# Optimization experiments

Hardware: AMD Instinct MI355X
Metric: run time of the kernel (lower is better)

The kernel has to match this reference:

```python
import jax, jax.numpy as jnp
import numpy as np

LN_ZERO = -100000000000.0
F_, D_, C_, V_ = 250000, 4, 2, 250000
E_ = F_ * D_
CD_ = C_ ** D_


def setup_inputs() -> dict:
    key = jax.random.key(0)
    k1, k2, k3 = jax.random.split(key, 3)
    # each factor has exactly D_ incident edges, one per variable slot
    edge_f = np.repeat(np.arange(E_ // D_ * 0 + F_ * 0 + F_)[:F_], D_)  # [E]
    pos = np.tile(np.arange(D_), F_)  # variable slot of each edge within its factor
    edge_v = np.asarray(jax.random.randint(k3, (E_,), 0, V_))
    # digit of each flat factor state along each axis: digits[k, s] in [0, C)
    state = np.arange(CD_)
    digits = (state[None, :] // (C_ ** (D_ - 1 - np.arange(D_)))[:, None]) % C_  # [D, CD]
    s_p = digits[pos]  # [E, CD]: the edge's own variable state within each factor state
    # permutation indices into the broadcast-first layout [E, C, C^(D-1)]
    scatter_idx = (np.arange(E_)[:, None] * CD_ + s_p * C_ ** (D_ - 1)).reshape(-1)
    fac_states_to_var = (np.arange(E_)[:, None] * C_ + s_p).reshape(-1)
    return {
        "prv_factorToVar_messages": jax.random.normal(k1, (E_, C_), jnp.float32),
        "factor_potentials": jax.random.normal(k2, (F_,) + (C_,) * D_, jnp.float32),
        "facToVar_edge_idx": jnp.asarray(np.stack([edge_f, edge_v]), jnp.int32),
        "facStates_to_varIdx": jnp.asarray(fac_states_to_var, jnp.int32),
        "varToFactorMsg_scatter_indices": jnp.asarray(scatter_idx, jnp.int32),
        "factor_potential_masks": jnp.zeros((F_,) + (C_,) * D_, jnp.int32),
        "factorToVar_messages_masks": jnp.zeros((E_, C_), bool),
        "varToFactor_messages_masks": jnp.zeros((E_, C_), bool),
        "var_beliefs_masks": jnp.zeros((V_, C_), bool),
    }


def _mask_clamp(x, mask):
    return jnp.maximum(jnp.where(mask, LN_ZERO, x), LN_ZERO)


def reference(prv_factorToVar_messages, factor_potentials, facToVar_edge_idx,
              facStates_to_varIdx, varToFactorMsg_scatter_indices,
              factor_potential_masks, factorToVar_messages_masks,
              varToFactor_messages_masks, var_beliefs_masks):
    E, C = prv_factorToVar_messages.shape
    F = factor_potentials.shape[0]
    V = var_beliefs_masks.shape[0]
    D = factor_potentials.ndim - 1
    edge_f, edge_v = facToVar_edge_idx[0], facToVar_edge_idx[1]

    def beliefs(msgs):
        vb = _mask_clamp(jax.ops.segment_sum(msgs, edge_v, num_segments=V), var_beliefs_masks)
        v2f = _mask_clamp(vb[edge_v] - msgs, varToFactor_messages_masks)
        # expanded[e, s] = v2f[e, s_p]; source is broadcast layout [E, C, C^(D-1)]
        expanded = v2f.reshape(-1)[varToFactorMsg_scatter_indices // (C ** (D - 1))]
        expanded = expanded.reshape((E,) + (C,) * D)
        fb = jax.ops.segment_sum(expanded.reshape(E, -1), edge_f, num_segments=F)
        fb = fb.reshape(factor_potentials.shape) + factor_potentials
        fb = jnp.maximum(jnp.where(factor_potential_masks == 1, LN_ZERO, fb), LN_ZERO)
        return vb, v2f, expanded, fb

    prv_vb, prv_v2f, exp_prv_v2f, prv_fb = beliefs(prv_factorToVar_messages)

    # new factor->var messages: max-marginalize (mode='map')
    nfv = prv_fb[edge_f] - exp_prv_v2f
    nfv = nfv - jnp.max(nfv)
    flat = nfv.reshape(-1)
    seg = jnp.where(facStates_to_varIdx >= 0, facStates_to_varIdx, E * C)  # invalid -> dropped slot
    new_f2v = jax.ops.segment_max(flat, seg, num_segments=E * C + 1)[:-1].reshape(E, C)
    # normalization: logsumexp over all dims except dim 0 (here just the state axis)
    new_f2v = new_f2v - jax.nn.logsumexp(new_f2v, axis=1, keepdims=True)
    new_f2v = _mask_clamp(new_f2v, factorToVar_messages_masks)

    vb, v2f, _, fb = beliefs(new_f2v)

    damping = 0.0
    f2v = _mask_clamp(damping * prv_factorToVar_messages + (1.0 - damping) * new_f2v,
                      factorToVar_messages_masks)
    return (f2v, vb, fb)
```

## Files before the change

kernel.cpp:

```cpp
#include <hip/hip_runtime.h>
#include <hip/hip_fp16.h>
#include <math.h>
#include <string.h>

#define LN_ZERO (-100000000000.0f)

constexpr int F_ = 250000;
constexpr int V_ = 250000;
constexpr int E_ = 1000000;

constexpr int NBLK  = 256;
constexpr int PARTS = 256;
constexpr int BINS  = 977;
constexpr int CAP   = 30;
constexpr int SLICE = (E_ + NBLK - 1) / NBLK;
constexpr int OVF_B = 1024;
constexpr int NWAVE = 16;
static_assert(PARTS * BINS >= V_, "");
static_assert(CAP <= 64, "segment items must fit one wave");
static_assert((size_t)NBLK * PARTS * CAP * 8 <= (size_t)F_ * 16 * 4, "buckets fit in out_fb");

static __device__ inline unsigned pack_h2(float x, float y) {
    __half2 h = __floats2half2_rn(x, y);
    unsigned u; memcpy(&u, &h, 4); return u;
}
static __device__ inline float2 unpack_h2(unsigned u) {
    __half2 h; memcpy(&h, &u, 4); return __half22float2(h);
}

__global__ __launch_bounds__(1024)
void k_ms1(const int* __restrict__ edge_v,
           const float2* __restrict__ msgs,
           const int4* __restrict__ potmask4,
           unsigned short* __restrict__ potbits,
           uint2* __restrict__ buckets,
           int* __restrict__ counts,
           uint2* __restrict__ ovf,
           int* __restrict__ ovf_counts) {
    __shared__ int cur[PARTS];
    __shared__ int ovf_cur;
    int b = blockIdx.x, tid = threadIdx.x;
    if (tid < PARTS) cur[tid] = 0;
    if (tid == 0) ovf_cur = 0;
    __syncthreads();

    int f = b * 1024 + tid;
    if (f < F_) {
        unsigned int bits = 0;
#pragma unroll
        for (int j = 0; j < 4; ++j) {
            int4 pm = potmask4[4 * f + j];
            bits |= (pm.x == 1 ? 1u : 0u) << (4 * j + 0);
            bits |= (pm.y == 1 ? 1u : 0u) << (4 * j + 1);
            bits |= (pm.z == 1 ? 1u : 0u) << (4 * j + 2);
            bits |= (pm.w == 1 ? 1u : 0u) << (4 * j + 3);
        }
        potbits[f] = (unsigned short)bits;
    }

    int ebase = b * SLICE;
    int eend = min(ebase + SLICE, E_);
    for (int e = ebase + tid; e < eend; e += 1024) {
        int v = edge_v[e];
        int p = v / BINS;
        float2 m = msgs[e];
        unsigned payload = pack_h2(m.x, m.y);
        int pos = atomicAdd(&cur[p], 1);
        if (pos < CAP) {
            buckets[((size_t)b * PARTS + p) * CAP + pos] =
                make_uint2((unsigned)(v - p * BINS), payload);
        } else {
            int op = atomicAdd(&ovf_cur, 1);
            if (op < OVF_B)
                ovf[(size_t)b * OVF_B + op] = make_uint2((unsigned)v, payload);
        }
    }
    __syncthreads();
    if (tid < PARTS) counts[b * PARTS + tid] = min(cur[tid], CAP);
    if (tid == 0) ovf_counts[b] = min(ovf_cur, OVF_B);
}

__global__ __launch_bounds__(1024)
void k_acc1(const uint2* __restrict__ buckets,
            const int* __restrict__ counts,
            const uint2* __restrict__ ovf,
            const int* __restrict__ ovf_counts,
            const unsigned short* __restrict__ vb_mask2,
            __half2* __restrict__ accP) {
    __shared__ float2 acc[BINS];
    __shared__ int ls_cnt[NBLK];
    __shared__ int ovfc[NBLK];
    int p = blockIdx.x, tid = threadIdx.x;
    int vbase = p * BINS;
    int nb = min(BINS, V_ - vbase);

    for (int j = tid; j < BINS; j += 1024) acc[j] = make_float2(0.f, 0.f);
    if (tid < NBLK) { ls_cnt[tid] = counts[tid * PARTS + p]; ovfc[tid] = ovf_counts[tid]; }
    __syncthreads();

    int wave = tid >> 6, lane = tid & 63;
    for (int b = wave; b < NBLK; b += NWAVE) {
        int n = ls_cnt[b];
        if (lane < n) {
            uint2 pr = buckets[((size_t)b * PARTS + p) * CAP + lane];
            float2 mv = unpack_h2(pr.y);
            atomicAdd(&acc[pr.x].x, mv.x);
            atomicAdd(&acc[pr.x].y, mv.y);
        }
    }
    for (int b = wave; b < NBLK; b += NWAVE) {
        int n = ovfc[b];
        for (int i = lane; i < n; i += 64) {
            uint2 pr = ovf[(size_t)b * OVF_B + i];
            int vl = (int)pr.x - vbase;
            if ((unsigned)vl < (unsigned)nb) {
                float2 mv = unpack_h2(pr.y);
                atomicAdd(&acc[vl].x, mv.x);
                atomicAdd(&acc[vl].y, mv.y);
            }
        }
    }
    __syncthreads();
    for (int j = tid; j < nb; j += 1024) {
        int v = vbase + j;
        unsigned short vbm = vb_mask2[v];
        float b0 = fmaxf((vbm & 0xff) ? LN_ZERO : acc[j].x, LN_ZERO);
        float b1 = fmaxf((vbm >> 8)   ? LN_ZERO : acc[j].y, LN_ZERO);
        accP[v] = __floats2half2_rn(b0, b1);
    }
}

__global__ void k_factor_msgs(const float2* __restrict__ msgs,
                              const int* __restrict__ edge_v,
                              const __half2* __restrict__ accP,
                              const float4* __restrict__ pot4,
                              const unsigned short* __restrict__ potbits,
                              const unsigned short* __restrict__ f2v_mask2,
                              const unsigned short* __restrict__ v2f_mask2,
                              float2* __restrict__ out_f2v) {
    int e = blockIdx.x * blockDim.x + threadIdx.x;
    if (e >= E_) return;
    int d = e & 3;
    int v = edge_v[e];

    float2 s = __half22float2(accP[v]);
    float2 m = msgs[e];
    unsigned short vm = v2f_mask2[e];
    float wx = fmaxf((vm & 0xff) ? LN_ZERO : (s.x - m.x), LN_ZERO);
    float wy = fmaxf((vm >> 8)   ? LN_ZERO : (s.y - m.y), LN_ZERO);

    float w0x = __shfl(wx, 0, 4), w0y = __shfl(wy, 0, 4);
    float w1x = __shfl(wx, 1, 4), w1y = __shfl(wy, 1, 4);
    float w2x = __shfl(wx, 2, 4), w2y = __shfl(wy, 2, 4);
    float w3x = __shfl(wx, 3, 4), w3y = __shfl(wy, 3, 4);

    float4 p = pot4[e];
    unsigned int pb = potbits[e >> 2] >> (4 * d);
    float A = ((d >> 1) ? w0y : w0x) + ((d & 1) ? w1y : w1x);
    float fb0 = p.x + A + w2x + w3x;
    float fb1 = p.y + A + w2x + w3y;
    float fb2 = p.z + A + w2y + w3x;
    float fb3 = p.w + A + w2y + w3y;
    fb0 = fmaxf((pb & 1u) ? LN_ZERO : fb0, LN_ZERO);
    fb1 = fmaxf((pb & 2u) ? LN_ZERO : fb1, LN_ZERO);
    fb2 = fmaxf((pb & 4u) ? LN_ZERO : fb2, LN_ZERO);
    fb3 = fmaxf((pb & 8u) ? LN_ZERO : fb3, LN_ZERO);

    float mk2_0 = fmaxf(fb0, fb1);
    float mk2_1 = fmaxf(fb2, fb3);
    float mk3_0 = fmaxf(fb0, fb2);
    float mk3_1 = fmaxf(fb1, fb3);
    float mloc  = fmaxf(mk2_0, mk2_1);

#pragma unroll
    for (int off = 1; off < 4; off <<= 1) {
        mk2_0 = fmaxf(mk2_0, __shfl_xor(mk2_0, off, 4));
        mk2_1 = fmaxf(mk2_1, __shfl_xor(mk2_1, off, 4));
        mk3_0 = fmaxf(mk3_0, __shfl_xor(mk3_0, off, 4));
        mk3_1 = fmaxf(mk3_1, __shfl_xor(mk3_1, off, 4));
    }
    float ml0 = __shfl(mloc, 0, 4);
    float ml1 = __shfl(mloc, 1, 4);
    float ml2 = __shfl(mloc, 2, 4);
    float ml3 = __shfl(mloc, 3, 4);

    float mm0, mm1;
    if (d == 0)      { mm0 = fmaxf(ml0, ml1); mm1 = fmaxf(ml2, ml3); }
    else if (d == 1) { mm0 = fmaxf(ml0, ml2); mm1 = fmaxf(ml1, ml3); }
    else if (d == 2) { mm0 = mk2_0;           mm1 = mk2_1; }
    else             { mm0 = mk3_0;           mm1 = mk3_1; }

    float raw0 = mm0 - wx;
    float raw1 = mm1 - wy;
    float mx = fmaxf(raw0, raw1);
    float lse = mx + logf(expf(raw0 - mx) + expf(raw1 - mx));
    unsigned short fm = f2v_mask2[e];
    float o0 = fmaxf((fm & 0xff) ? LN_ZERO : (raw0 - lse), LN_ZERO);
    float o1 = fmaxf((fm >> 8)   ? LN_ZERO : (raw1 - lse), LN_ZERO);
    out_f2v[e] = make_float2(o0, o1);
}

__global__ __launch_bounds__(1024)
void k_ms2(const int* __restrict__ edge_v,
           const float2* __restrict__ f2v,
           uint2* __restrict__ buckets,
           int* __restrict__ counts,
           uint2* __restrict__ ovf,
           int* __restrict__ ovf_counts) {
    __shared__ int cur[PARTS];
    __shared__ int ovf_cur;
    int b = blockIdx.x, tid = threadIdx.x;
    if (tid < PARTS) cur[tid] = 0;
    if (tid == 0) ovf_cur = 0;
    __syncthreads();
    int ebase = b * SLICE;
    int eend = min(ebase + SLICE, E_);
    for (int e = ebase + tid; e < eend; e += 1024) {
        int v = edge_v[e];
        int p = v / BINS;
        float2 g = f2v[e];
        unsigned payload = pack_h2(g.x, g.y);
        int pos = atomicAdd(&cur[p], 1);
        if (pos < CAP) {
            buckets[((size_t)b * PARTS + p) * CAP + pos] =
                make_uint2((unsigned)(v - p * BINS), payload);
        } else {
            int op = atomicAdd(&ovf_cur, 1);
            if (op < OVF_B)
                ovf[(size_t)b * OVF_B + op] = make_uint2((unsigned)v, payload);
        }
    }
    __syncthreads();
    if (tid < PARTS) counts[b * PARTS + tid] = min(cur[tid], CAP);
    if (tid == 0) ovf_counts[b] = min(ovf_cur, OVF_B);
}

__global__ __launch_bounds__(1024)
void k_acc2(const uint2* __restrict__ buckets,
            const int* __restrict__ counts,
            const uint2* __restrict__ ovf,
            const int* __restrict__ ovf_counts,
            const unsigned short* __restrict__ vb_mask2,
            float2* __restrict__ out_vb,
            __half2* __restrict__ accN) {
    __shared__ float2 acc[BINS];
    __shared__ int ls_cnt[NBLK];
    __shared__ int ovfc[NBLK];
    int p = blockIdx.x, tid = threadIdx.x;
    int vbase = p * BINS;
    int nb = min(BINS, V_ - vbase);

    for (int j = tid; j < BINS; j += 1024) acc[j] = make_float2(0.f, 0.f);
    if (tid < NBLK) { ls_cnt[tid] = counts[tid * PARTS + p]; ovfc[tid] = ovf_counts[tid]; }
    __syncthreads();

    int wave = tid >> 6, lane = tid & 63;
    for (int b = wave; b < NBLK; b += NWAVE) {
        int n = ls_cnt[b];
        if (lane < n) {
            uint2 pr = buckets[((size_t)b * PARTS + p) * CAP + lane];
            float2 mv = unpack_h2(pr.y);
            atomicAdd(&acc[pr.x].x, mv.x);
            atomicAdd(&acc[pr.x].y, mv.y);
        }
    }
    for (int b = wave; b < NBLK; b += NWAVE) {
        int n = ovfc[b];
        for (int i = lane; i < n; i += 64) {
            uint2 pr = ovf[(size_t)b * OVF_B + i];
            int vl = (int)pr.x - vbase;
            if ((unsigned)vl < (unsigned)nb) {
                float2 mv = unpack_h2(pr.y);
                atomicAdd(&acc[vl].x, mv.x);
                atomicAdd(&acc[vl].y, mv.y);
            }
        }
    }
    __syncthreads();
    for (int j = tid; j < nb; j += 1024) {
        int v = vbase + j;
        unsigned short vbm = vb_mask2[v];
        float b0 = fmaxf((vbm & 0xff) ? LN_ZERO : acc[j].x, LN_ZERO);
        float b1 = fmaxf((vbm >> 8)   ? LN_ZERO : acc[j].y, LN_ZERO);
        out_vb[v] = make_float2(b0, b1);
        accN[v] = __floats2half2_rn(b0, b1);
    }
}

__global__ void k_factor_beliefs(const float2* __restrict__ new_f2v,
                                 const __half2* __restrict__ accN,
                                 const int* __restrict__ edge_v,
                                 const float4* __restrict__ pot4,
                                 const unsigned short* __restrict__ potbits,
                                 const unsigned short* __restrict__ v2f_mask2,
                                 float4* __restrict__ out_fb4) {
    int e = blockIdx.x * blockDim.x + threadIdx.x;
    if (e >= E_) return;
    int d = e & 3;

    float2 b = __half22float2(accN[edge_v[e]]);
    float2 g = new_f2v[e];
    unsigned short vm = v2f_mask2[e];
    float wx = fmaxf((vm & 0xff) ? LN_ZERO : (b.x - g.x), LN_ZERO);
    float wy = fmaxf((vm >> 8)   ? LN_ZERO : (b.y - g.y), LN_ZERO);

    float w0x = __shfl(wx, 0, 4), w0y = __shfl(wy, 0, 4);
    float w1x = __shfl(wx, 1, 4), w1y = __shfl(wy, 1, 4);
    float w2x = __shfl(wx, 2, 4), w2y = __shfl(wy, 2, 4);
    float w3x = __shfl(wx, 3, 4), w3y = __shfl(wy, 3, 4);

    float4 p = pot4[e];
    unsigned int pb = potbits[e >> 2] >> (4 * d);
    float A = ((d >> 1) ? w0y : w0x) + ((d & 1) ? w1y : w1x);
    float o0 = fmaxf((pb & 1u) ? LN_ZERO : (p.x + A + w2x + w3x), LN_ZERO);
    float o1 = fmaxf((pb & 2u) ? LN_ZERO : (p.y + A + w2x + w3y), LN_ZERO);
    float o2 = fmaxf((pb & 4u) ? LN_ZERO : (p.z + A + w2y + w3x), LN_ZERO);
    float o3 = fmaxf((pb & 8u) ? LN_ZERO : (p.w + A + w2y + w3y), LN_ZERO);
    out_fb4[e] = make_float4(o0, o1, o2, o3);
}

extern "C" void kernel_launch(void* const* d_in, const int* in_sizes, int n_in,
                              void* d_out, int out_size, void* d_ws, size_t ws_size,
                              hipStream_t stream) {
    const float* msgs     = (const float*)d_in[0];
    const float* pot      = (const float*)d_in[1];
    const int*   edge_idx = (const int*)d_in[2];
    const int*   pot_mask = (const int*)d_in[5];
    const unsigned char* f2v_mask = (const unsigned char*)d_in[6];
    const unsigned char* v2f_mask = (const unsigned char*)d_in[7];
    const unsigned char* vb_mask  = (const unsigned char*)d_in[8];

    const int* edge_v = edge_idx + E_;

    float* out      = (float*)d_out;
    float* out_f2v  = out;
    float* out_vb   = out + (size_t)E_ * 2;
    float* out_fb   = out_vb + (size_t)V_ * 2;

    uint2* buckets = (uint2*)out_fb;

    int* counts = (int*)d_ws;
    int* ovf_counts = counts + NBLK * PARTS;
    uint2* ovf = (uint2*)(ovf_counts + NBLK);
    __half2* accP = (__half2*)(ovf + (size_t)NBLK * OVF_B);
    __half2* accN = accP + V_;
    unsigned short* potbits = (unsigned short*)(accN + V_);

    const int B = 256;
    dim3 gE((E_ + B - 1) / B);

    k_ms1<<<NBLK, 1024, 0, stream>>>(edge_v, (const float2*)msgs,
                                     (const int4*)pot_mask, potbits,
                                     buckets, counts, ovf, ovf_counts);
    k_acc1<<<PARTS, 1024, 0, stream>>>(buckets, counts, ovf, ovf_counts,
                                       (const unsigned short*)vb_mask, accP);

    k_factor_msgs<<<gE, B, 0, stream>>>((const float2*)msgs, edge_v, accP,
                                        (const float4*)pot, potbits,
                                        (const unsigned short*)f2v_mask,
                                        (const unsigned short*)v2f_mask,
                                        (float2*)out_f2v);

    k_ms2<<<NBLK, 1024, 0, stream>>>(edge_v, (const float2*)out_f2v,
                                     buckets, counts, ovf, ovf_counts);
    k_acc2<<<PARTS, 1024, 0, stream>>>(buckets, counts, ovf, ovf_counts,
                                       (const unsigned short*)vb_mask,
                                       (float2*)out_vb, accN);

    k_factor_beliefs<<<gE, B, 0, stream>>>((const float2*)out_f2v, accN, edge_v,
                                           (const float4*)pot, potbits,
                                           (const unsigned short*)v2f_mask,
                                           (float4*)out_fb);
}
```

Measured before the change: 77.66 us.

## Fuse factor-message compute into second bucket-scatter kernel and transpose counts layout

Merges the per-edge factor-to-variable message kernel into the second partitioning/bucket kernel, so the new messages are scattered into buckets straight from registers instead of being reread from global memory. This removes one launch and one read of out_f2v. SLICE is set to a multiple of 4 so each factor's four edges fall in the same block and wave group for the width-4 shuffles. The counts array becomes partition-major, so each accumulate block reads its counts contiguously. The fused kernel runs only 256 blocks of 1024 threads, down from about 3900 blocks of 256, which may cut parallelism and latency hiding for the compute-heavy part.

```diff
diff --git a/kernel.cpp b/kernel.cpp
--- a/kernel.cpp
+++ b/kernel.cpp
@@ -13,10 +13,12 @@
 constexpr int PARTS = 256;
 constexpr int BINS  = 977;
 constexpr int CAP   = 30;
-constexpr int SLICE = (E_ + NBLK - 1) / NBLK;
+constexpr int SLICE = 3908;
 constexpr int OVF_B = 1024;
 constexpr int NWAVE = 16;
 static_assert(PARTS * BINS >= V_, "");
+static_assert((size_t)NBLK * SLICE >= E_, "");
+static_assert(SLICE % 4 == 0, "");
 static_assert(CAP <= 64, "segment items must fit one wave");
 static_assert((size_t)NBLK * PARTS * CAP * 8 <= (size_t)F_ * 16 * 4, "buckets fit in out_fb");
 
@@ -76,7 +78,7 @@
         }
     }
     __syncthreads();
-    if (tid < PARTS) counts[b * PARTS + tid] = min(cur[tid], CAP);
+    if (tid < PARTS) counts[tid * NBLK + b] = min(cur[tid], CAP);
     if (tid == 0) ovf_counts[b] = min(ovf_cur, OVF_B);
 }
 
@@ -95,7 +97,7 @@
     int nb = min(BINS, V_ - vbase);
 
     for (int j = tid; j < BINS; j += 1024) acc[j] = make_float2(0.f, 0.f);
-    if (tid < NBLK) { ls_cnt[tid] = counts[tid * PARTS + p]; ovfc[tid] = ovf_counts[tid]; }
+    if (tid < NBLK) { ls_cnt[tid] = counts[p * NBLK + tid]; ovfc[tid] = ovf_counts[tid]; }
     __syncthreads();
 
     int wave = tid >> 6, lane = tid & 63;
@@ -130,100 +132,94 @@
     }
 }
 
-__global__ void k_factor_msgs(const float2* __restrict__ msgs,
-                              const int* __restrict__ edge_v,
-                              const __half2* __restrict__ accP,
-                              const float4* __restrict__ pot4,
-                              const unsigned short* __restrict__ potbits,
-                              const unsigned short* __restrict__ f2v_mask2,
-                              const unsigned short* __restrict__ v2f_mask2,
-                              float2* __restrict__ out_f2v) {
-    int e = blockIdx.x * blockDim.x + threadIdx.x;
-    if (e >= E_) return;
-    int d = e & 3;
-    int v = edge_v[e];
-
-    float2 s = __half22float2(accP[v]);
-    float2 m = msgs[e];
-    unsigned short vm = v2f_mask2[e];
-    float wx = fmaxf((vm & 0xff) ? LN_ZERO : (s.x - m.x), LN_ZERO);
-    float wy = fmaxf((vm >> 8)   ? LN_ZERO : (s.y - m.y), LN_ZERO);
-
-    float w0x = __shfl(wx, 0, 4), w0y = __shfl(wy, 0, 4);
-    float w1x = __shfl(wx, 1, 4), w1y = __shfl(wy, 1, 4);
-    float w2x = __shfl(wx, 2, 4), w2y = __shfl(wy, 2, 4);
-    float w3x = __shfl(wx, 3, 4), w3y = __shfl(wy, 3, 4);
-
-    float4 p = pot4[e];
-    unsigned int pb = potbits[e >> 2] >> (4 * d);
-    float A = ((d >> 1) ? w0y : w0x) + ((d & 1) ? w1y : w1x);
-    float fb0 = p.x + A + w2x + w3x;
-    float fb1 = p.y + A + w2x + w3y;
-    float fb2 = p.z + A + w2y + w3x;
-    float fb3 = p.w + A + w2y + w3y;
-    fb0 = fmaxf((pb & 1u) ? LN_ZERO : fb0, LN_ZERO);
-    fb1 = fmaxf((pb & 2u) ? LN_ZERO : fb1, LN_ZERO);
-    fb2 = fmaxf((pb & 4u) ? LN_ZERO : fb2, LN_ZERO);
-    fb3 = fmaxf((pb & 8u) ? LN_ZERO : fb3, LN_ZERO);
-
-    float mk2_0 = fmaxf(fb0, fb1);
-    float mk2_1 = fmaxf(fb2, fb3);
-    float mk3_0 = fmaxf(fb0, fb2);
-    float mk3_1 = fmaxf(fb1, fb3);
-    float mloc  = fmaxf(mk2_0, mk2_1);
-
-#pragma unroll
-    for (int off = 1; off < 4; off <<= 1) {
-        mk2_0 = fmaxf(mk2_0, __shfl_xor(mk2_0, off, 4));
-        mk2_1 = fmaxf(mk2_1, __shfl_xor(mk2_1, off, 4));
-        mk3_0 = fmaxf(mk3_0, __shfl_xor(mk3_0, off, 4));
-        mk3_1 = fmaxf(mk3_1, __shfl_xor(mk3_1, off, 4));
-    }
-    float ml0 = __shfl(mloc, 0, 4);
-    float ml1 = __shfl(mloc, 1, 4);
-    float ml2 = __shfl(mloc, 2, 4);
-    float ml3 = __shfl(mloc, 3, 4);
-
-    float mm0, mm1;
-    if (d == 0)      { mm0 = fmaxf(ml0, ml1); mm1 = fmaxf(ml2, ml3); }
-    else if (d == 1) { mm0 = fmaxf(ml0, ml2); mm1 = fmaxf(ml1, ml3); }
-    else if (d == 2) { mm0 = mk2_0;           mm1 = mk2_1; }
-    else             { mm0 = mk3_0;           mm1 = mk3_1; }
-
-    float raw0 = mm0 - wx;
-    float raw1 = mm1 - wy;
-    float mx = fmaxf(raw0, raw1);
-    float lse = mx + logf(expf(raw0 - mx) + expf(raw1 - mx));
-    unsigned short fm = f2v_mask2[e];
-    float o0 = fmaxf((fm & 0xff) ? LN_ZERO : (raw0 - lse), LN_ZERO);
-    float o1 = fmaxf((fm >> 8)   ? LN_ZERO : (raw1 - lse), LN_ZERO);
-    out_f2v[e] = make_float2(o0, o1);
-}
-
 __global__ __launch_bounds__(1024)
-void k_ms2(const int* __restrict__ edge_v,
-           const float2* __restrict__ f2v,
-           uint2* __restrict__ buckets,
-           int* __restrict__ counts,
-           uint2* __restrict__ ovf,
-           int* __restrict__ ovf_counts) {
+void k_fm_ms2(const float2* __restrict__ msgs,
+              const int* __restrict__ edge_v,
+              const __half2* __restrict__ accP,
+              const float4* __restrict__ pot4,
+              const unsigned short* __restrict__ potbits,
+              const unsigned short* __restrict__ f2v_mask2,
+              const unsigned short* __restrict__ v2f_mask2,
+              float2* __restrict__ out_f2v,
+              uint2* __restrict__ buckets,
+              int* __restrict__ counts,
+              uint2* __restrict__ ovf,
+              int* __restrict__ ovf_counts) {
     __shared__ int cur[PARTS];
     __shared__ int ovf_cur;
     int b = blockIdx.x, tid = threadIdx.x;
     if (tid < PARTS) cur[tid] = 0;
     if (tid == 0) ovf_cur = 0;
     __syncthreads();
+
     int ebase = b * SLICE;
     int eend = min(ebase + SLICE, E_);
     for (int e = ebase + tid; e < eend; e += 1024) {
+        int d = e & 3;
         int v = edge_v[e];
-        int p = v / BINS;
-        float2 g = f2v[e];
-        unsigned payload = pack_h2(g.x, g.y);
-        int pos = atomicAdd(&cur[p], 1);
+
+        float2 s = __half22float2(accP[v]);
+        float2 m = msgs[e];
+        unsigned short vm = v2f_mask2[e];
+        float wx = fmaxf((vm & 0xff) ? LN_ZERO : (s.x - m.x), LN_ZERO);
+        float wy = fmaxf((vm >> 8)   ? LN_ZERO : (s.y - m.y), LN_ZERO);
+
+        float w0x = __shfl(wx, 0, 4), w0y = __shfl(wy, 0, 4);
+        float w1x = __shfl(wx, 1, 4), w1y = __shfl(wy, 1, 4);
+        float w2x = __shfl(wx, 2, 4), w2y = __shfl(wy, 2, 4);
+        float w3x = __shfl(wx, 3, 4), w3y = __shfl(wy, 3, 4);
+
+        float4 p = pot4[e];
+        unsigned int pb = potbits[e >> 2] >> (4 * d);
+        float A = ((d >> 1) ? w0y : w0x) + ((d & 1) ? w1y : w1x);
+        float fb0 = p.x + A + w2x + w3x;
+        float fb1 = p.y + A + w2x + w3y;
+        float fb2 = p.z + A + w2y + w3x;
+        float fb3 = p.w + A + w2y + w3y;
+        fb0 = fmaxf((pb & 1u) ? LN_ZERO : fb0, LN_ZERO);
+        fb1 = fmaxf((pb & 2u) ? LN_ZERO : fb1, LN_ZERO);
+        fb2 = fmaxf((pb & 4u) ? LN_ZERO : fb2, LN_ZERO);
+        fb3 = fmaxf((pb & 8u) ? LN_ZERO : fb3, LN_ZERO);
+
+        float mk2_0 = fmaxf(fb0, fb1);
+        float mk2_1 = fmaxf(fb2, fb3);
+        float mk3_0 = fmaxf(fb0, fb2);
+        float mk3_1 = fmaxf(fb1, fb3);
+        float mloc  = fmaxf(mk2_0, mk2_1);
+
+#pragma unroll
+        for (int off = 1; off < 4; off <<= 1) {
+            mk2_0 = fmaxf(mk2_0, __shfl_xor(mk2_0, off, 4));
+            mk2_1 = fmaxf(mk2_1, __shfl_xor(mk2_1, off, 4));
+            mk3_0 = fmaxf(mk3_0, __shfl_xor(mk3_0, off, 4));
+            mk3_1 = fmaxf(mk3_1, __shfl_xor(mk3_1, off, 4));
+        }
+        float ml0 = __shfl(mloc, 0, 4);
+        float ml1 = __shfl(mloc, 1, 4);
+        float ml2 = __shfl(mloc, 2, 4);
+        float ml3 = __shfl(mloc, 3, 4);
+
+        float mm0, mm1;
+        if (d == 0)      { mm0 = fmaxf(ml0, ml1); mm1 = fmaxf(ml2, ml3); }
+        else if (d == 1) { mm0 = fmaxf(ml0, ml2); mm1 = fmaxf(ml1, ml3); }
+        else if (d == 2) { mm0 = mk2_0;           mm1 = mk2_1; }
+        else             { mm0 = mk3_0;           mm1 = mk3_1; }
+
+        float raw0 = mm0 - wx;
+        float raw1 = mm1 - wy;
+        float mx = fmaxf(raw0, raw1);
+        float lse = mx + logf(expf(raw0 - mx) + expf(raw1 - mx));
+        unsigned short fm = f2v_mask2[e];
+        float o0 = fmaxf((fm & 0xff) ? LN_ZERO : (raw0 - lse), LN_ZERO);
+        float o1 = fmaxf((fm >> 8)   ? LN_ZERO : (raw1 - lse), LN_ZERO);
+        out_f2v[e] = make_float2(o0, o1);
+
+        int pp = v / BINS;
+        unsigned payload = pack_h2(o0, o1);
+        int pos = atomicAdd(&cur[pp], 1);
         if (pos < CAP) {
-            buckets[((size_t)b * PARTS + p) * CAP + pos] =
-                make_uint2((unsigned)(v - p * BINS), payload);
+            buckets[((size_t)b * PARTS + pp) * CAP + pos] =
+                make_uint2((unsigned)(v - pp * BINS), payload);
         } else {
             int op = atomicAdd(&ovf_cur, 1);
             if (op < OVF_B)
@@ -231,7 +227,7 @@
         }
     }
     __syncthreads();
-    if (tid < PARTS) counts[b * PARTS + tid] = min(cur[tid], CAP);
+    if (tid < PARTS) counts[tid * NBLK + b] = min(cur[tid], CAP);
     if (tid == 0) ovf_counts[b] = min(ovf_cur, OVF_B);
 }
 
@@ -251,7 +247,7 @@
     int nb = min(BINS, V_ - vbase);
 
     for (int j = tid; j < BINS; j += 1024) acc[j] = make_float2(0.f, 0.f);
-    if (tid < NBLK) { ls_cnt[tid] = counts[tid * PARTS + p]; ovfc[tid] = ovf_counts[tid]; }
+    if (tid < NBLK) { ls_cnt[tid] = counts[p * NBLK + tid]; ovfc[tid] = ovf_counts[tid]; }
     __syncthreads();
 
     int wave = tid >> 6, lane = tid & 63;
@@ -355,14 +351,13 @@
     k_acc1<<<PARTS, 1024, 0, stream>>>(buckets, counts, ovf, ovf_counts,
                                        (const unsigned short*)vb_mask, accP);
 
-    k_factor_msgs<<<gE, B, 0, stream>>>((const float2*)msgs, edge_v, accP,
+    k_fm_ms2<<<NBLK, 1024, 0, stream>>>((const float2*)msgs, edge_v, accP,
                                         (const float4*)pot, potbits,
                                         (const unsigned short*)f2v_mask,
                                         (const unsigned short*)v2f_mask,
-                                        (float2*)out_f2v);
-
-    k_ms2<<<NBLK, 1024, 0, stream>>>(edge_v, (const float2*)out_f2v,
-                                     buckets, counts, ovf, ovf_counts);
+                                        (float2*)out_f2v,
+                                        buckets, counts, ovf, ovf_counts);
+
     k_acc2<<<PARTS, 1024, 0, stream>>>(buckets, counts, ovf, ovf_counts,
                                        (const unsigned short*)vb_mask,
                                        (float2*)out_vb, accN);
```

New measurement: 75.00 us. 1.04x faster.
